# Kernel tuning notes

Hardware: AMD Instinct MI355X
Metric: run time of the kernel (lower is better)

## Reference

```python
import jax, jax.numpy as jnp
import numpy as np

B, S = 2, 2048
HID = 2560
NH, NKV, HD = 20, 5, 128
GROUPS = NH // NKV  # 4
THETA = 500000.0
RMS_EPS = 1e-6  # RMSNorm default eps used for attn_sub_norm
NEG_INF = -1e9


def pack_ternary(key, M, K):
    """Pack ternary weights {-1,0,1} (stored as trits {0,1,2}) into SIMD
    block-interleaved uint8 layout: per 128-elem block, byte j holds
    weights j+0 (bits 6:7), j+32 (4:5), j+64 (2:3), j+96 (0:1)."""
    t = jax.random.randint(key, (M, K), 0, 3).astype(jnp.uint8)
    t = t.reshape(M, K // 128, 4, 32)
    byte = (t[:, :, 0] << 6) | (t[:, :, 1] << 4) | (t[:, :, 2] << 2) | t[:, :, 3]
    return byte.reshape(M, K // 4)


def unpack_ternary(packed):
    """Inverse of pack_ternary -> float weights in {-1,0,1}. (M, K//4) -> (M, K)."""
    M, Kp = packed.shape
    nb = Kp // 32
    b = packed.reshape(M, nb, 32)
    fields = jnp.stack([(b >> 6) & 3, (b >> 4) & 3, (b >> 2) & 3, b & 3], axis=2)
    return fields.reshape(M, nb * 128).astype(jnp.float32) - 1.0


def bitlinear(x, packed, scale):
    w = unpack_ternary(packed) * scale  # (out, in)
    return jnp.einsum('bsi,oi->bso', x, w)


def rotate_half(x):
    h = x.shape[-1] // 2
    return jnp.concatenate([-x[..., h:], x[..., :h]], axis=-1)


def rms_norm(x, w, eps=RMS_EPS):
    var = jnp.mean(jnp.square(x.astype(jnp.float32)), axis=-1, keepdims=True)
    return (w * (x * jax.lax.rsqrt(var + eps))).astype(x.dtype)


def setup_inputs() -> dict:
    key = jax.random.key(0)
    ks = jax.random.split(key, 6)
    hidden_states = jax.random.normal(ks[0], (B, S, HID), dtype=jnp.float32)
    causal = jnp.tril(jnp.ones((S, S), dtype=bool))
    attention_mask = jnp.where(causal, 0.0, NEG_INF).astype(jnp.float32)[None, None]
    return {
        'hidden_states': hidden_states,
        'attention_mask': attention_mask,
        'q_w': pack_ternary(ks[1], NH * HD, HID),
        'k_w': pack_ternary(ks[2], NKV * HD, HID),
        'v_w': pack_ternary(ks[3], NKV * HD, HID),
        'o_w': pack_ternary(ks[4], HID, NH * HD),
        'q_scale': jnp.float32(0.02),
        'k_scale': jnp.float32(0.02),
        'v_scale': jnp.float32(0.02),
        'o_scale': jnp.float32(0.02),
        'attn_norm_w': jnp.ones((NH * HD,), dtype=jnp.float32),
    }


def reference(hidden_states, attention_mask, q_w, k_w, v_w, o_w,
              q_scale, k_scale, v_scale, o_scale, attn_norm_w):
    bsz, seq_len, _ = hidden_states.shape
    q = bitlinear(hidden_states, q_w, q_scale)
    k = bitlinear(hidden_states, k_w, k_scale)
    v = bitlinear(hidden_states, v_w, v_scale)
    q = q.reshape(bsz, seq_len, NH, HD).transpose(0, 2, 1, 3)    # (b,h,s,d)
    k = k.reshape(bsz, seq_len, NKV, HD).transpose(0, 2, 1, 3)
    v = v.reshape(bsz, seq_len, NKV, HD).transpose(0, 2, 1, 3)
    # rotary embedding
    inv_freq = 1.0 / (THETA ** (jnp.arange(0, HD, 2, dtype=jnp.float32) / HD))
    t = jnp.arange(seq_len, dtype=jnp.float32)
    freqs = t[:, None] * inv_freq[None, :]            # (s, d/2)
    emb = jnp.concatenate([freqs, freqs], axis=-1)    # (s, d)
    cos, sin = jnp.cos(emb), jnp.sin(emb)
    q = q * cos + rotate_half(q) * sin
    k = k * cos + rotate_half(k) * sin
    # GQA: repeat kv heads
    k = jnp.repeat(k, GROUPS, axis=1)
    v = jnp.repeat(v, GROUPS, axis=1)
    scores = jnp.einsum('bhqd,bhkd->bhqk', q, k) / np.sqrt(HD).astype(np.float32)
    scores = scores + attention_mask
    attn = jax.nn.softmax(scores.astype(jnp.float32), axis=-1).astype(q.dtype)
    out = jnp.einsum('bhqk,bhkd->bhqd', attn, v)
    out = out.transpose(0, 2, 1, 3).reshape(bsz, seq_len, NH * HD)
    out = rms_norm(out, attn_norm_w)
    return bitlinear(out, o_w, o_scale)
```

## Files before the change

kernel.cpp:

```cpp
#include <hip/hip_runtime.h>
#include <cstdint>
#include <cstddef>

typedef __bf16 bf16x8 __attribute__((ext_vector_type(8)));
typedef float  f32x4  __attribute__((ext_vector_type(4)));
typedef int    i32x4  __attribute__((ext_vector_type(4)));
typedef unsigned short u16x4 __attribute__((ext_vector_type(4)));

#define DEV __device__ __forceinline__
#define NEGINF (-__builtin_inff())

DEV uint16_t f2bf(float f) {
  union { float f; uint32_t u; } v; v.f = f;
  uint32_t u = v.u;
  u += 0x7FFFu + ((u >> 16) & 1u);
  return (uint16_t)(u >> 16);
}
DEV float bf2f(uint16_t h) {
  union { uint32_t u; float f; } v; v.u = ((uint32_t)h) << 16;
  return v.f;
}

DEV void gload_lds16(const void* g, void* l) {
  __builtin_amdgcn_global_load_lds(
      (const __attribute__((address_space(1))) void*)g,
      (__attribute__((address_space(3))) void*)l, 16, 0, 0);
}


__global__ void k_f32_to_bf16(const float* __restrict__ in, uint16_t* __restrict__ out, int n4) {
  int i = blockIdx.x * blockDim.x + threadIdx.x;
  if (i >= n4) return;
  f32x4 v = *(const f32x4*)(in + (size_t)i * 4);
  u16x4 o;
  o[0] = f2bf(v[0]); o[1] = f2bf(v[1]); o[2] = f2bf(v[2]); o[3] = f2bf(v[3]);
  *(u16x4*)(out + (size_t)i * 4) = o;
}

__global__ void k_unpack(const uint32_t* __restrict__ p, uint16_t* __restrict__ w, int total, int Kq) {
  int idx = blockIdx.x * blockDim.x + threadIdx.x;
  if (idx >= total) return;
  int row = idx / Kq, pc = idx - row * Kq;
  int blk = pc >> 5, j = pc & 31;
  uint32_t b = p[idx] & 0xFFu;
  size_t base = (size_t)row * (size_t)(Kq * 4) + (size_t)blk * 128 + j;
  w[base]      = f2bf((float)((b >> 6) & 3u) - 1.0f);
  w[base + 32] = f2bf((float)((b >> 4) & 3u) - 1.0f);
  w[base + 64] = f2bf((float)((b >> 2) & 3u) - 1.0f);
  w[base + 96] = f2bf((float)(b & 3u) - 1.0f);
}

__global__ void k_rope_table(float* __restrict__ cosT, float* __restrict__ sinT) {
  int idx = blockIdx.x * blockDim.x + threadIdx.x;
  int s = idx >> 6, i = idx & 63;
  float inv = expf((float)i * (-13.122363377404328f / 64.0f));
  float fr = (float)s * inv;
  cosT[idx] = cosf(fr);
  sinT[idx] = sinf(fr);
}

__global__ void k_rope(uint16_t* __restrict__ buf, const float* __restrict__ cosT,
                       const float* __restrict__ sinT, int H, int total) {
  int idx = blockIdx.x * blockDim.x + threadIdx.x;
  if (idx >= total) return;
  int d = idx & 63;
  int t = idx >> 6;
  int h = t % H;
  int row = t / H;
  int s = row & 2047;
  size_t base = (size_t)row * (size_t)(H * 128) + (size_t)h * 128 + d;
  float x1 = bf2f(buf[base]), x2 = bf2f(buf[base + 64]);
  float c = cosT[(s << 6) + d], sn = sinT[(s << 6) + d];
  buf[base]      = f2bf(x1 * c - x2 * sn);
  buf[base + 64] = f2bf(x2 * c + x1 * sn);
}

template<int MODE>
__global__ __launch_bounds__(256, 2)
void k_gemm(const uint16_t* __restrict__ A, const uint16_t* __restrict__ W,
            uint16_t* __restrict__ Qo, uint16_t* __restrict__ Ko, uint16_t* __restrict__ Vo,
            float* __restrict__ Fo,
            const float* __restrict__ s0p, const float* __restrict__ s1p, const float* __restrict__ s2p,
            int M, int N, int K)
{
  __shared__ uint16_t As[128 * 64];
  __shared__ uint16_t Bs[128 * 64];
  const int tid = threadIdx.x;
  const int n0 = blockIdx.x * 128, m0 = blockIdx.y * 128;
  const int lane = tid & 63, w = tid >> 6;
  const int wm = (w >> 1) * 64, wn = (w & 1) * 64;
  const int lr = lane & 15, lg = lane >> 4, lk = lg * 8;
  const size_t K2 = (size_t)K * 2;
  f32x4 acc[4][4] = {};

  const int srow = tid >> 3;
  const int cprime = ((tid & 7) * 16) ^ ((srow & 7) << 4);
  const uint8_t* Ag = (const uint8_t*)A + (size_t)(m0 + srow) * K2 + cprime;
  const uint8_t* Wg = (const uint8_t*)W + (size_t)(n0 + srow) * K2 + cprime;
  char* Al = (char*)As + w * 1024;
  char* Bl = (char*)Bs + w * 1024;

  for (size_t k0b = 0; k0b < K2; k0b += 128) {
    #pragma unroll
    for (int i = 0; i < 4; ++i)
      gload_lds16(Ag + (size_t)(i * 32) * K2 + k0b, Al + i * 4096);
    #pragma unroll
    for (int i = 0; i < 4; ++i)
      gload_lds16(Wg + (size_t)(i * 32) * K2 + k0b, Bl + i * 4096);
    __syncthreads();
    #pragma unroll
    for (int kc = 0; kc < 64; kc += 32) {
      bf16x8 a[4], b[4];
      #pragma unroll
      for (int i = 0; i < 4; ++i) {
        const int r = wm + i * 16 + lr;
        a[i] = *(const bf16x8*)((const char*)As + r * 128 + (((kc + lk) * 2) ^ ((r & 7) << 4)));
      }
      #pragma unroll
      for (int j = 0; j < 4; ++j) {
        const int r = wn + j * 16 + lr;
        b[j] = *(const bf16x8*)((const char*)Bs + r * 128 + (((kc + lk) * 2) ^ ((r & 7) << 4)));
      }
      #pragma unroll
      for (int i = 0; i < 4; ++i)
        #pragma unroll
        for (int j = 0; j < 4; ++j)
          acc[i][j] = __builtin_amdgcn_mfma_f32_16x16x32_bf16(a[i], b[j], acc[i][j], 0, 0, 0);
    }
    __syncthreads();
  }

  if (MODE == 0) {
    const float qs = *s0p, ks = *s1p, vs = *s2p;
    #pragma unroll
    for (int i = 0; i < 4; ++i) {
      const int rowb = m0 + wm + i * 16 + lg * 4;
      #pragma unroll
      for (int j = 0; j < 4; ++j) {
        const int col = n0 + wn + j * 16 + lr;
        #pragma unroll
        for (int r = 0; r < 4; ++r) {
          const int rr = rowb + r;
          const float v = acc[i][j][r];
          if (col < 2560) {
            Qo[(size_t)rr * 2560 + col] = f2bf(v * qs);
          } else if (col < 3200) {
            Ko[(size_t)rr * 640 + (col - 2560)] = f2bf(v * ks);
          } else {
            const int n2 = col - 3200;
            const int kvh = n2 >> 7, d = n2 & 127;
            const int bb = rr >> 11, ss = rr & 2047;
            Vo[(((size_t)(bb * 5 + kvh) * 128 + d) << 11) + ss] = f2bf(v * vs);
          }
        }
      }
    }
  } else {
    const float os = *s0p;
    #pragma unroll
    for (int i = 0; i < 4; ++i) {
      const int rowb = m0 + wm + i * 16 + lg * 4;
      #pragma unroll
      for (int j = 0; j < 4; ++j) {
        const int col = n0 + wn + j * 16 + lr;
        #pragma unroll
        for (int r = 0; r < 4; ++r)
          Fo[(size_t)(rowb + r) * N + col] = acc[i][j][r] * os;
      }
    }
  }
}

__global__ __launch_bounds__(256)
void k_attn(const uint16_t* __restrict__ Q, const uint16_t* __restrict__ Kb,
            const uint16_t* __restrict__ Vt, uint16_t* __restrict__ Ob)
{
  __shared__ char Klds[2][16384];
  __shared__ char Vlds[2][16384];
  __shared__ uint16_t p_lds[4][16][88];

  const int lin = blockIdx.x;
  const int gslot = (lin & 7) * 160 + (lin >> 3);
  const int bk = gslot >> 7;
  const int st = 127 - (gslot & 127);
  const int b = bk / 5, kvh = bk - b * 5;

  const int tid = threadIdx.x, lane = tid & 63, w = tid >> 6;
  const int lr = lane & 15, lg = lane >> 4, lk = lg * 8;
  const int h = kvh * 4 + w;
  uint16_t (*pl)[88] = p_lds[w];
  const int kswz = (lr & 7) << 4;

  const uint8_t* Kg = (const uint8_t*)(Kb + (size_t)b * 2048 * 640 + (size_t)kvh * 128);
  const uint8_t* Vg = (const uint8_t*)(Vt + ((size_t)(b * 5 + kvh) * 128) * 2048);

  const int krow = tid >> 4;
  const int kcol = ((tid & 15) * 16) ^ ((krow & 7) << 4);
  const int vrow = tid >> 3;
  const int vcol = ((tid & 7) * 16) ^ ((vrow & 7) << 4);
  const int dst16 = tid * 16;

  const float C = 0.127531019577f;

  const int q0 = st * 16;
  const int ns = (q0 + 79) >> 6;

  bf16x8 qf[4];
  {
    const size_t qbase = ((size_t)(b * 2048 + q0 + lr)) * 2560 + (size_t)h * 128 + lk;
    #pragma unroll
    for (int c = 0; c < 4; ++c) qf[c] = *(const bf16x8*)&Q[qbase + c * 32];
  }

  {
    const uint8_t* Ks = Kg + (size_t)krow * 1280 + kcol;
    const uint8_t* Vs = Vg + (size_t)vrow * 4096 + vcol;
    #pragma unroll
    for (int i = 0; i < 4; ++i) gload_lds16(Ks + (size_t)i * 16 * 1280, Klds[0] + dst16 + i * 4096);
    #pragma unroll
    for (int i = 0; i < 4; ++i) gload_lds16(Vs + (size_t)i * 32 * 4096, Vlds[0] + dst16 + i * 4096);
  }

  int cur = 0;
  float m = NEGINF, l = 0.f;
  f32x4 oa[8] = {};

  #pragma unroll 1
  for (int stp = 0; stp < ns; ++stp) {
    const int k0 = stp * 64;
    __syncthreads();

    if (stp + 1 < ns) {
      const int kn = k0 + 64;
      const uint8_t* Ks = Kg + (size_t)(kn + krow) * 1280 + kcol;
      const uint8_t* Vs = Vg + (size_t)vrow * 4096 + (size_t)kn * 2 + vcol;
      char* Kd = Klds[cur ^ 1] + dst16;
      char* Vd = Vlds[cur ^ 1] + dst16;
      #pragma unroll
      for (int i = 0; i < 4; ++i) gload_lds16(Ks + (size_t)i * 16 * 1280, Kd + i * 4096);
      #pragma unroll
      for (int i = 0; i < 4; ++i) gload_lds16(Vs + (size_t)i * 32 * 4096, Vd + i * 4096);
    }

    const char* Kc = Klds[cur];
    const char* Vc = Vlds[cur];
    const bool bound = (k0 + 64 >= q0 + 16);

    __builtin_amdgcn_s_setprio(1);
    f32x4 sa[4] = {};
    #pragma unroll
    for (int t = 0; t < 4; ++t) {
      #pragma unroll
      for (int c = 0; c < 4; ++c) {
        bf16x8 kf = *(const bf16x8*)(Kc + (t * 16 + lr) * 256 + ((c * 64 + lg * 16) ^ kswz));
        sa[t] = __builtin_amdgcn_mfma_f32_16x16x32_bf16(kf, qf[c], sa[t], 0, 0, 0);
      }
    }
    __builtin_amdgcn_s_setprio(0);

    float u[16];
    if (bound) {
      #pragma unroll
      for (int t = 0; t < 4; ++t)
        #pragma unroll
        for (int r = 0; r < 4; ++r)
          u[t * 4 + r] = (k0 + t * 16 + lg * 4 + r <= q0 + lr) ? sa[t][r] * C : NEGINF;
    } else {
      #pragma unroll
      for (int t = 0; t < 4; ++t)
        #pragma unroll
        for (int r = 0; r < 4; ++r)
          u[t * 4 + r] = sa[t][r] * C;
    }
    float m01 = fmaxf(u[0], u[1]),   m23 = fmaxf(u[2], u[3]);
    float m45 = fmaxf(u[4], u[5]),   m67 = fmaxf(u[6], u[7]);
    float m89 = fmaxf(u[8], u[9]),   mab = fmaxf(u[10], u[11]);
    float mcd = fmaxf(u[12], u[13]), mef = fmaxf(u[14], u[15]);
    float mx = fmaxf(fmaxf(fmaxf(m01, m23), fmaxf(m45, m67)),
                     fmaxf(fmaxf(m89, mab), fmaxf(mcd, mef)));
    mx = fmaxf(mx, __shfl_xor(mx, 16));
    mx = fmaxf(mx, __shfl_xor(mx, 32));
    const float mn = fmaxf(m, mx);
    const float resc = __builtin_exp2f(m - mn);
    m = mn;
    float pv[16];
    #pragma unroll
    for (int i = 0; i < 16; ++i) pv[i] = __builtin_exp2f(u[i] - mn);
    float s0 = (pv[0] + pv[1]) + (pv[2] + pv[3]);
    float s1 = (pv[4] + pv[5]) + (pv[6] + pv[7]);
    float s2 = (pv[8] + pv[9]) + (pv[10] + pv[11]);
    float s3 = (pv[12] + pv[13]) + (pv[14] + pv[15]);
    l = l * resc + ((s0 + s1) + (s2 + s3));
    #pragma unroll
    for (int t = 0; t < 4; ++t) {
      union { __bf16 b4[4]; unsigned long long u64; } pk;
      #pragma unroll
      for (int r = 0; r < 4; ++r) pk.b4[r] = (__bf16)pv[t * 4 + r];
      *(unsigned long long*)&pl[lr][t * 16 + lg * 4] = pk.u64;
    }
    #pragma unroll
    for (int dc = 0; dc < 8; ++dc) {
      oa[dc][0] *= resc; oa[dc][1] *= resc; oa[dc][2] *= resc; oa[dc][3] *= resc;
    }
    bf16x8 pa0 = *(const bf16x8*)&pl[lr][lk];
    bf16x8 pa1 = *(const bf16x8*)&pl[lr][32 + lk];
    __builtin_amdgcn_s_setprio(1);
    #pragma unroll
    for (int dc = 0; dc < 8; ++dc) {
      bf16x8 vf0 = *(const bf16x8*)(Vc + (dc * 16 + lr) * 128 + ((lg * 16) ^ kswz));
      bf16x8 vf1 = *(const bf16x8*)(Vc + (dc * 16 + lr) * 128 + ((64 + lg * 16) ^ kswz));
      oa[dc] = __builtin_amdgcn_mfma_f32_16x16x32_bf16(vf0, pa0, oa[dc], 0, 0, 0);
      oa[dc] = __builtin_amdgcn_mfma_f32_16x16x32_bf16(vf1, pa1, oa[dc], 0, 0, 0);
    }
    __builtin_amdgcn_s_setprio(0);
    cur ^= 1;
  }

  float lf = l;
  lf += __shfl_xor(lf, 16);
  lf += __shfl_xor(lf, 32);
  const float inv = 1.0f / lf;
  const size_t obase = ((size_t)(b * 2048 + q0 + lr)) * 2560 + (size_t)h * 128;
  #pragma unroll
  for (int dc = 0; dc < 8; ++dc) {
    union { __bf16 b4[4]; unsigned long long u64; } ok;
    #pragma unroll
    for (int r = 0; r < 4; ++r) ok.b4[r] = (__bf16)(oa[dc][r] * inv);
    *(unsigned long long*)&Ob[obase + dc * 16 + lg * 4] = ok.u64;
  }
}

__global__ __launch_bounds__(256)
void k_rmsnorm(const uint16_t* __restrict__ X, const float* __restrict__ g, uint16_t* __restrict__ Y)
{
  const int row = blockIdx.x;
  const int tid = threadIdx.x;
  const uint16_t* x = X + (size_t)row * 2560;
  float ss = 0.f;
  #pragma unroll
  for (int it = 0; it < 10; ++it) {
    const int i = tid + it * 256;
    const float v = bf2f(x[i]);
    ss += v * v;
  }
  #pragma unroll
  for (int off = 1; off < 64; off <<= 1) ss += __shfl_xor(ss, off, 64);
  __shared__ float sred[4];
  if ((tid & 63) == 0) sred[tid >> 6] = ss;
  __syncthreads();
  const float tot = sred[0] + sred[1] + sred[2] + sred[3];
  const float rs = rsqrtf(tot * (1.0f / 2560.0f) + 1e-6f);
  uint16_t* y = Y + (size_t)row * 2560;
  #pragma unroll
  for (int it = 0; it < 10; ++it) {
    const int i = tid + it * 256;
    y[i] = f2bf(bf2f(x[i]) * rs * g[i]);
  }
}

extern "C" void kernel_launch(void* const* d_in, const int* in_sizes, int n_in,
                              void* d_out, int out_size, void* d_ws, size_t ws_size,
                              hipStream_t stream)
{
  const float*    x     = (const float*)d_in[0];
  const uint32_t* qw    = (const uint32_t*)d_in[2];
  const uint32_t* kw    = (const uint32_t*)d_in[3];
  const uint32_t* vw    = (const uint32_t*)d_in[4];
  const uint32_t* ow    = (const uint32_t*)d_in[5];
  const float*    qs    = (const float*)d_in[6];
  const float*    ks    = (const float*)d_in[7];
  const float*    vs    = (const float*)d_in[8];
  const float*    os    = (const float*)d_in[9];
  const float*    gnorm = (const float*)d_in[10];

  char* ws = (char*)d_ws;
  uint16_t* xb   = (uint16_t*)(ws + 0);
  uint16_t* wqkv = (uint16_t*)(ws + 20971520);
  uint16_t* owb  = (uint16_t*)(ws + 40632320);
  float*    cosT = (float*)   (ws + 53739520);
  float*    sinT = (float*)   (ws + 54263808);
  uint16_t* Qb   = (uint16_t*)(ws + 54788096);
  uint16_t* Kb   = (uint16_t*)(ws + 75759616);
  uint16_t* Vt   = (uint16_t*)(ws + 81002496);

  k_f32_to_bf16<<<10240, 256, 0, stream>>>(x, xb, 2621440);
  k_unpack<<<6400, 256, 0, stream>>>(qw, wqkv, 1638400, 640);
  k_unpack<<<1600, 256, 0, stream>>>(kw, wqkv + (size_t)2560 * 2560, 409600, 640);
  k_unpack<<<1600, 256, 0, stream>>>(vw, wqkv + (size_t)3200 * 2560, 409600, 640);
  k_unpack<<<6400, 256, 0, stream>>>(ow, owb, 1638400, 640);
  k_rope_table<<<512, 256, 0, stream>>>(cosT, sinT);

  k_gemm<0><<<dim3(30, 32), 256, 0, stream>>>(xb, wqkv, Qb, Kb, Vt, nullptr,
                                              qs, ks, vs, 4096, 3840, 2560);
  k_rope<<<20480, 256, 0, stream>>>(Qb, cosT, sinT, 20, 5242880);
  k_rope<<<5120, 256, 0, stream>>>(Kb, cosT, sinT, 5, 1310720);

  k_attn<<<dim3(1280), 256, 0, stream>>>(Qb, Kb, Vt, xb);

  k_rmsnorm<<<4096, 256, 0, stream>>>(xb, gnorm, Qb);

  k_gemm<1><<<dim3(20, 32), 256, 0, stream>>>(Qb, owb, nullptr, nullptr, nullptr,
                                              (float*)d_out, os, nullptr, nullptr,
                                              4096, 2560, 2560);
}
```

Before: 335.5 us.

## Process two 16-row query tiles per attention wave to reuse K/V tiles

Each wave in the attention kernel now handles 32 query rows as two 16-row groups, holding two sets of Q fragments, accumulators and softmax state. Every K/V tile loaded into LDS is used for twice as many queries, and the grid shrinks from 1280 to 640 blocks. The intent is to halve K/V global traffic and LDS fragment reads per query. The costs are higher register pressure (a launch bound of 2 blocks is added), fewer blocks to cover the causal load imbalance, and a slightly smaller padded P buffer in LDS.

```diff
diff --git a/kernel.cpp b/kernel.cpp
--- a/kernel.cpp
+++ b/kernel.cpp
@@ -171,24 +171,24 @@
   }
 }
 
-__global__ __launch_bounds__(256)
+__global__ __launch_bounds__(256, 2)
 void k_attn(const uint16_t* __restrict__ Q, const uint16_t* __restrict__ Kb,
             const uint16_t* __restrict__ Vt, uint16_t* __restrict__ Ob)
 {
   __shared__ char Klds[2][16384];
   __shared__ char Vlds[2][16384];
-  __shared__ uint16_t p_lds[4][16][88];
+  __shared__ uint16_t p_lds[4][16][72];
 
   const int lin = blockIdx.x;
-  const int gslot = (lin & 7) * 160 + (lin >> 3);
-  const int bk = gslot >> 7;
-  const int st = 127 - (gslot & 127);
+  const int gslot = (lin & 7) * 80 + (lin >> 3);
+  const int bk = gslot >> 6;
+  const int st = 63 - (gslot & 63);
   const int b = bk / 5, kvh = bk - b * 5;
 
   const int tid = threadIdx.x, lane = tid & 63, w = tid >> 6;
   const int lr = lane & 15, lg = lane >> 4, lk = lg * 8;
   const int h = kvh * 4 + w;
-  uint16_t (*pl)[88] = p_lds[w];
+  uint16_t (*pl)[72] = p_lds[w];
   const int kswz = (lr & 7) << 4;
 
   const uint8_t* Kg = (const uint8_t*)(Kb + (size_t)b * 2048 * 640 + (size_t)kvh * 128);
@@ -202,14 +202,17 @@
 
   const float C = 0.127531019577f;
 
-  const int q0 = st * 16;
-  const int ns = (q0 + 79) >> 6;
-
-  bf16x8 qf[4];
+  const int q0 = st * 32;
+  const int ns = (q0 + 95) >> 6;
+
+  bf16x8 qf0[4], qf1[4];
   {
-    const size_t qbase = ((size_t)(b * 2048 + q0 + lr)) * 2560 + (size_t)h * 128 + lk;
-    #pragma unroll
-    for (int c = 0; c < 4; ++c) qf[c] = *(const bf16x8*)&Q[qbase + c * 32];
+    const size_t qb0 = ((size_t)(b * 2048 + q0 + lr)) * 2560 + (size_t)h * 128 + lk;
+    #pragma unroll
+    for (int c = 0; c < 4; ++c) {
+      qf0[c] = *(const bf16x8*)&Q[qb0 + c * 32];
+      qf1[c] = *(const bf16x8*)&Q[qb0 + 16 * 2560 + c * 32];
+    }
   }
 
   {
@@ -222,8 +225,8 @@
   }
 
   int cur = 0;
-  float m = NEGINF, l = 0.f;
-  f32x4 oa[8] = {};
+  float m0 = NEGINF, m1 = NEGINF, l0 = 0.f, l1 = 0.f;
+  f32x4 oa0[8] = {}, oa1[8] = {};
 
   #pragma unroll 1
   for (int stp = 0; stp < ns; ++stp) {
@@ -244,89 +247,102 @@
 
     const char* Kc = Klds[cur];
     const char* Vc = Vlds[cur];
-    const bool bound = (k0 + 64 >= q0 + 16);
 
     __builtin_amdgcn_s_setprio(1);
-    f32x4 sa[4] = {};
+    f32x4 sa0[4] = {}, sa1[4] = {};
     #pragma unroll
     for (int t = 0; t < 4; ++t) {
       #pragma unroll
       for (int c = 0; c < 4; ++c) {
         bf16x8 kf = *(const bf16x8*)(Kc + (t * 16 + lr) * 256 + ((c * 64 + lg * 16) ^ kswz));
-        sa[t] = __builtin_amdgcn_mfma_f32_16x16x32_bf16(kf, qf[c], sa[t], 0, 0, 0);
+        sa0[t] = __builtin_amdgcn_mfma_f32_16x16x32_bf16(kf, qf0[c], sa0[t], 0, 0, 0);
+        sa1[t] = __builtin_amdgcn_mfma_f32_16x16x32_bf16(kf, qf1[c], sa1[t], 0, 0, 0);
       }
     }
     __builtin_amdgcn_s_setprio(0);
 
-    float u[16];
-    if (bound) {
-      #pragma unroll
-      for (int t = 0; t < 4; ++t)
-        #pragma unroll
-        for (int r = 0; r < 4; ++r)
-          u[t * 4 + r] = (k0 + t * 16 + lg * 4 + r <= q0 + lr) ? sa[t][r] * C : NEGINF;
-    } else {
-      #pragma unroll
-      for (int t = 0; t < 4; ++t)
-        #pragma unroll
-        for (int r = 0; r < 4; ++r)
-          u[t * 4 + r] = sa[t][r] * C;
-    }
-    float m01 = fmaxf(u[0], u[1]),   m23 = fmaxf(u[2], u[3]);
-    float m45 = fmaxf(u[4], u[5]),   m67 = fmaxf(u[6], u[7]);
-    float m89 = fmaxf(u[8], u[9]),   mab = fmaxf(u[10], u[11]);
-    float mcd = fmaxf(u[12], u[13]), mef = fmaxf(u[14], u[15]);
-    float mx = fmaxf(fmaxf(fmaxf(m01, m23), fmaxf(m45, m67)),
-                     fmaxf(fmaxf(m89, mab), fmaxf(mcd, mef)));
-    mx = fmaxf(mx, __shfl_xor(mx, 16));
-    mx = fmaxf(mx, __shfl_xor(mx, 32));
-    const float mn = fmaxf(m, mx);
-    const float resc = __builtin_exp2f(m - mn);
-    m = mn;
-    float pv[16];
-    #pragma unroll
-    for (int i = 0; i < 16; ++i) pv[i] = __builtin_exp2f(u[i] - mn);
-    float s0 = (pv[0] + pv[1]) + (pv[2] + pv[3]);
-    float s1 = (pv[4] + pv[5]) + (pv[6] + pv[7]);
-    float s2 = (pv[8] + pv[9]) + (pv[10] + pv[11]);
-    float s3 = (pv[12] + pv[13]) + (pv[14] + pv[15]);
-    l = l * resc + ((s0 + s1) + (s2 + s3));
-    #pragma unroll
-    for (int t = 0; t < 4; ++t) {
-      union { __bf16 b4[4]; unsigned long long u64; } pk;
-      #pragma unroll
-      for (int r = 0; r < 4; ++r) pk.b4[r] = (__bf16)pv[t * 4 + r];
-      *(unsigned long long*)&pl[lr][t * 16 + lg * 4] = pk.u64;
-    }
+    #pragma unroll
+    for (int g = 0; g < 2; ++g) {
+      const f32x4* sa = g ? sa1 : sa0;
+      f32x4* oa = g ? oa1 : oa0;
+      float& m = g ? m1 : m0;
+      float& l = g ? l1 : l0;
+      const int q0g = q0 + 16 * g;
+
+      float u[16];
+      if (k0 + 63 > q0g) {
+        #pragma unroll
+        for (int t = 0; t < 4; ++t)
+          #pragma unroll
+          for (int r = 0; r < 4; ++r)
+            u[t * 4 + r] = (k0 + t * 16 + lg * 4 + r <= q0g + lr) ? sa[t][r] * C : NEGINF;
+      } else {
+        #pragma unroll
+        for (int t = 0; t < 4; ++t)
+          #pragma unroll
+          for (int r = 0; r < 4; ++r)
+            u[t * 4 + r] = sa[t][r] * C;
+      }
+      float m01 = fmaxf(u[0], u[1]),   m23 = fmaxf(u[2], u[3]);
+      float m45 = fmaxf(u[4], u[5]),   m67 = fmaxf(u[6], u[7]);
+      float m89 = fmaxf(u[8], u[9]),   mab = fmaxf(u[10], u[11]);
+      float mcd = fmaxf(u[12], u[13]), mef = fmaxf(u[14], u[15]);
+      float mx = fmaxf(fmaxf(fmaxf(m01, m23), fmaxf(m45, m67)),
+                       fmaxf(fmaxf(m89, mab), fmaxf(mcd, mef)));
+      mx = fmaxf(mx, __shfl_xor(mx, 16));
+      mx = fmaxf(mx, __shfl_xor(mx, 32));
+      const float mn = fmaxf(m, mx);
+      const float resc = __builtin_exp2f(m - mn);
+      m = mn;
+      float pv[16];
+      #pragma unroll
+      for (int i = 0; i < 16; ++i) pv[i] = __builtin_exp2f(u[i] - mn);
+      float s0 = (pv[0] + pv[1]) + (pv[2] + pv[3]);
+      float s1 = (pv[4] + pv[5]) + (pv[6] + pv[7]);
+      float s2 = (pv[8] + pv[9]) + (pv[10] + pv[11]);
+      float s3 = (pv[12] + pv[13]) + (pv[14] + pv[15]);
+      l = l * resc + ((s0 + s1) + (s2 + s3));
+      #pragma unroll
+      for (int t = 0; t < 4; ++t) {
+        union { __bf16 b4[4]; unsigned long long u64; } pk;
+        #pragma unroll
+        for (int r = 0; r < 4; ++r) pk.b4[r] = (__bf16)pv[t * 4 + r];
+        *(unsigned long long*)&pl[lr][t * 16 + lg * 4] = pk.u64;
+      }
+      #pragma unroll
+      for (int dc = 0; dc < 8; ++dc) {
+        oa[dc][0] *= resc; oa[dc][1] *= resc; oa[dc][2] *= resc; oa[dc][3] *= resc;
+      }
+      bf16x8 pa0 = *(const bf16x8*)&pl[lr][lk];
+      bf16x8 pa1 = *(const bf16x8*)&pl[lr][32 + lk];
+      __builtin_amdgcn_s_setprio(1);
+      #pragma unroll
+      for (int dc = 0; dc < 8; ++dc) {
+        bf16x8 vf0 = *(const bf16x8*)(Vc + (dc * 16 + lr) * 128 + ((lg * 16) ^ kswz));
+        bf16x8 vf1 = *(const bf16x8*)(Vc + (dc * 16 + lr) * 128 + ((64 + lg * 16) ^ kswz));
+        oa[dc] = __builtin_amdgcn_mfma_f32_16x16x32_bf16(vf0, pa0, oa[dc], 0, 0, 0);
+        oa[dc] = __builtin_amdgcn_mfma_f32_16x16x32_bf16(vf1, pa1, oa[dc], 0, 0, 0);
+      }
+      __builtin_amdgcn_s_setprio(0);
+    }
+    cur ^= 1;
+  }
+
+  #pragma unroll
+  for (int g = 0; g < 2; ++g) {
+    f32x4* oa = g ? oa1 : oa0;
+    float lf = g ? l1 : l0;
+    lf += __shfl_xor(lf, 16);
+    lf += __shfl_xor(lf, 32);
+    const float inv = 1.0f / lf;
+    const size_t obase = ((size_t)(b * 2048 + q0 + 16 * g + lr)) * 2560 + (size_t)h * 128;
     #pragma unroll
     for (int dc = 0; dc < 8; ++dc) {
-      oa[dc][0] *= resc; oa[dc][1] *= resc; oa[dc][2] *= resc; oa[dc][3] *= resc;
-    }
-    bf16x8 pa0 = *(const bf16x8*)&pl[lr][lk];
-    bf16x8 pa1 = *(const bf16x8*)&pl[lr][32 + lk];
-    __builtin_amdgcn_s_setprio(1);
-    #pragma unroll
-    for (int dc = 0; dc < 8; ++dc) {
-      bf16x8 vf0 = *(const bf16x8*)(Vc + (dc * 16 + lr) * 128 + ((lg * 16) ^ kswz));
-      bf16x8 vf1 = *(const bf16x8*)(Vc + (dc * 16 + lr) * 128 + ((64 + lg * 16) ^ kswz));
-      oa[dc] = __builtin_amdgcn_mfma_f32_16x16x32_bf16(vf0, pa0, oa[dc], 0, 0, 0);
-      oa[dc] = __builtin_amdgcn_mfma_f32_16x16x32_bf16(vf1, pa1, oa[dc], 0, 0, 0);
-    }
-    __builtin_amdgcn_s_setprio(0);
-    cur ^= 1;
-  }
-
-  float lf = l;
-  lf += __shfl_xor(lf, 16);
-  lf += __shfl_xor(lf, 32);
-  const float inv = 1.0f / lf;
-  const size_t obase = ((size_t)(b * 2048 + q0 + lr)) * 2560 + (size_t)h * 128;
-  #pragma unroll
-  for (int dc = 0; dc < 8; ++dc) {
-    union { __bf16 b4[4]; unsigned long long u64; } ok;
-    #pragma unroll
-    for (int r = 0; r < 4; ++r) ok.b4[r] = (__bf16)(oa[dc][r] * inv);
-    *(unsigned long long*)&Ob[obase + dc * 16 + lg * 4] = ok.u64;
+      union { __bf16 b4[4]; unsigned long long u64; } ok;
+      #pragma unroll
+      for (int r = 0; r < 4; ++r) ok.b4[r] = (__bf16)(oa[dc][r] * inv);
+      *(unsigned long long*)&Ob[obase + dc * 16 + lg * 4] = ok.u64;
+    }
   }
 }
 
@@ -395,7 +411,7 @@
   k_rope<<<20480, 256, 0, stream>>>(Qb, cosT, sinT, 20, 5242880);
   k_rope<<<5120, 256, 0, stream>>>(Kb, cosT, sinT, 5, 1310720);
 
-  k_attn<<<dim3(1280), 256, 0, stream>>>(Qb, Kb, Vt, xb);
+  k_attn<<<dim3(640), 256, 0, stream>>>(Qb, Kb, Vt, xb);
 
   k_rmsnorm<<<4096, 256, 0, stream>>>(xb, gnorm, Qb);
 
```

After: 316.2 us. -5.8%, faster.
